# Kernel optimization log

Measured on AMD Instinct MI355X. Metric: run time of the kernel, lower is better.

The kernel has to match this reference:

```python
import jax, jax.numpy as jnp
import numpy as np

B, S, Hd, NH, FF = 4, 2048, 1024, 16, 4096
D = Hd // NH  # head size 64
EPS = 1e-12


def _ln(x, g, b):
    mu = jnp.mean(x, axis=-1, keepdims=True)
    var = jnp.mean(jnp.square(x - mu), axis=-1, keepdims=True)
    return (x - mu) * jax.lax.rsqrt(var + EPS) * g + b


def _rope(q, k):
    # q,k: [B,NH,S,D]; RoFormer interleaved rotary
    inv = 1.0 / (10000.0 ** (jnp.arange(0, D, 2, dtype=jnp.float32) / D))
    freqs = jnp.arange(S, dtype=jnp.float32)[:, None] * inv[None, :]  # [S,D/2]
    cos = jnp.repeat(jnp.cos(freqs), 2, axis=-1)  # [S,D]
    sin = jnp.repeat(jnp.sin(freqs), 2, axis=-1)

    def rot(x):  # [x0,x1,x2,x3,...] -> [-x1,x0,-x3,x2,...]
        return jnp.stack([-x[..., 1::2], x[..., 0::2]], axis=-1).reshape(x.shape)

    return q * cos + rot(q) * sin, k * cos + rot(k) * sin


def setup_inputs() -> dict:
    key = jax.random.key(0)
    ks = jax.random.split(key, 12)
    s = 0.02
    return {
        "x": jax.random.normal(ks[0], (B, S, Hd), jnp.float32),
        "Wq": jax.random.normal(ks[1], (Hd, Hd), jnp.float32) * s,
        "bq": jnp.zeros((Hd,), jnp.float32),
        "Wk": jax.random.normal(ks[2], (Hd, Hd), jnp.float32) * s,
        "bk": jnp.zeros((Hd,), jnp.float32),
        "Wv": jax.random.normal(ks[3], (Hd, Hd), jnp.float32) * s,
        "bv": jnp.zeros((Hd,), jnp.float32),
        "Wo": jax.random.normal(ks[4], (Hd, Hd), jnp.float32) * s,
        "bo": jnp.zeros((Hd,), jnp.float32),
        "g1": jnp.ones((Hd,), jnp.float32),
        "beta1": jnp.zeros((Hd,), jnp.float32),
        "W1": jax.random.normal(ks[5], (Hd, FF), jnp.float32) * s,
        "b1": jnp.zeros((FF,), jnp.float32),
        "W2": jax.random.normal(ks[6], (FF, Hd), jnp.float32) * s,
        "b2": jnp.zeros((Hd,), jnp.float32),
        "g2": jnp.ones((Hd,), jnp.float32),
        "beta2": jnp.zeros((Hd,), jnp.float32),
    }


def reference(x, Wq, bq, Wk, bk, Wv, bv, Wo, bo, g1, beta1, W1, b1, W2, b2, g2, beta2):
    def proj(W, b):  # [B,S,Hd] -> [B,NH,S,D]
        return (x @ W + b).reshape(B, S, NH, D).transpose(0, 2, 1, 3)

    q, k, v = proj(Wq, bq), proj(Wk, bk), proj(Wv, bv)
    q, k = _rope(q, k)
    scores = jnp.einsum('bhqd,bhkd->bhqk', q, k) / jnp.sqrt(jnp.float32(D))
    attn = jax.nn.softmax(scores, axis=-1)
    ctx = jnp.einsum('bhqk,bhkd->bhqd', attn, v)
    ctx = ctx.transpose(0, 2, 1, 3).reshape(B, S, Hd)
    attn_out = ctx @ Wo + bo
    h = _ln(x + attn_out, g1, beta1)
    ffn = jax.nn.gelu(h @ W1 + b1) @ W2 + b2
    return _ln(h + ffn, g2, beta2)
```

## Files before the change

### kernel.cpp

```cpp
#include <hip/hip_runtime.h>

#define BB   4
#define SS   2048
#define HD   1024
#define NHH  16
#define DD   64
#define FFF  4096
#define BS   (BB*SS)
#define BHN  (BB*NHH)

typedef __attribute__((ext_vector_type(8))) short v8s;
typedef __attribute__((ext_vector_type(4))) short v4s;
typedef __attribute__((ext_vector_type(4))) float v4f;

__device__ __forceinline__ short f2bf(float f) {
    union { float f; unsigned u; } v; v.f = f;
    unsigned r = (v.u + 0x7fffu + ((v.u >> 16) & 1u)) >> 16;
    return (short)r;
}
__device__ __forceinline__ float bf2f(short s) {
    union { unsigned u; float f; } v; v.u = ((unsigned)(unsigned short)s) << 16;
    return v.f;
}
__device__ __forceinline__ unsigned pktrunc(float lo, float hi) {
    return __builtin_amdgcn_perm(__builtin_bit_cast(unsigned, hi),
                                 __builtin_bit_cast(unsigned, lo), 0x07060302u);
}
__device__ __forceinline__ v4f mfma16(v8s a, v8s b, v4f c) {
    return __builtin_amdgcn_mfma_f32_16x16x32_bf16(a, b, c, 0, 0, 0);
}
__device__ __forceinline__ void cp16(void* lds, const void* g) {
    __builtin_amdgcn_global_load_lds(
        (const __attribute__((address_space(1))) unsigned*)g,
        (__attribute__((address_space(3))) unsigned*)lds, 16, 0, 0);
}


__global__ __launch_bounds__(256) void cast_bf16(const float* __restrict__ X,
                                                 short* __restrict__ Y, int n) {
    const int i = (blockIdx.x * 256 + threadIdx.x) * 4;
    if (i < n) {
        const float4 v = *(const float4*)(X + i);
        v4s o = { f2bf(v.x), f2bf(v.y), f2bf(v.z), f2bf(v.w) };
        *(v4s*)(Y + i) = o;
    }
}

__global__ __launch_bounds__(256) void rope_tab(float* __restrict__ C, float* __restrict__ Sn) {
    const int i = blockIdx.x * 256 + threadIdx.x;
    const int s = i >> 5, di = i & 31;
    const float inv = powf(10000.f, -(float)(2 * di) * (1.f / 64.f));
    const float a = (float)s * inv;
    C[i]  = cosf(a);
    Sn[i] = sinf(a);
}

__global__ __launch_bounds__(256) void transW(const float* __restrict__ W,
                                              short* __restrict__ WT, int K, int N) {
    __shared__ float T[64][65];
    const int t = threadIdx.x;
    const int r0 = blockIdx.y * 64, c0 = blockIdx.x * 64;
#pragma unroll
    for (int i = 0; i < 4; i++) {
        const int lin = t + 256 * i;
        const int r = lin >> 4, c = (lin & 15) * 4;
        const float4 v = *(const float4*)(W + (size_t)(r0 + r) * N + c0 + c);
        T[r][c] = v.x; T[r][c+1] = v.y; T[r][c+2] = v.z; T[r][c+3] = v.w;
    }
    __syncthreads();
#pragma unroll
    for (int i = 0; i < 4; i++) {
        const int lin = t + 256 * i;
        const int n = lin >> 4, k = (lin & 15) * 4;
        v4s o = { f2bf(T[k][n]), f2bf(T[k+1][n]), f2bf(T[k+2][n]), f2bf(T[k+3][n]) };
        *(v4s*)(WT + (size_t)(c0 + n) * K + r0 + k) = o;
    }
}


template <int EPI>
__global__ __launch_bounds__(256, 2) void gemm_bt(
    const short* __restrict__ A, const short* __restrict__ Bt,
    const float* __restrict__ bias, const float* __restrict__ bias2,
    const float* __restrict__ bias3, void* __restrict__ out,
    void* __restrict__ out2,
    const float* __restrict__ ropeC, const float* __restrict__ ropeS,
    int M, int N, int K, float oscale)
{
    __shared__ short As[128 * 32];
    __shared__ short Bs[128 * 32];
    const int t = threadIdx.x;
    const int wave = t >> 6, lane = t & 63;
    const int quad = lane >> 4, l16 = lane & 15;
    const int wm = wave & 1, wn = wave >> 1;
    const int m0 = blockIdx.x * 128, n0 = blockIdx.y * 128;

    v4f acc[4][4];
#pragma unroll
    for (int i = 0; i < 4; i++)
#pragma unroll
        for (int j = 0; j < 4; j++) { v4f z = {0.f, 0.f, 0.f, 0.f}; acc[i][j] = z; }

    const int r4 = lane >> 2;
    const int g4 = (lane & 3) ^ ((lane >> 3) & 3);
    const short* Asrc = A  + (size_t)(m0 + wave * 32 + r4) * K + g4 * 8;
    const short* Bsrc = Bt + (size_t)(n0 + wave * 32 + r4) * K + g4 * 8;
    short* Adst = As + wave * 1024;
    short* Bdst = Bs + wave * 1024;
    const int pshift = (l16 >> 1) & 3;

    for (int k0 = 0; k0 < K; k0 += 32) {
        __syncthreads();
        cp16(Adst,       Asrc + k0);
        cp16(Adst + 512, Asrc + (size_t)16 * K + k0);
        cp16(Bdst,       Bsrc + k0);
        cp16(Bdst + 512, Bsrc + (size_t)16 * K + k0);
        __syncthreads();
        v8s af[4], bfr[4];
#pragma unroll
        for (int i = 0; i < 4; i++)
            af[i] = *(const v8s*)(As + (wm * 64 + i * 16 + l16) * 32 + (quad ^ pshift) * 8);
#pragma unroll
        for (int j = 0; j < 4; j++)
            bfr[j] = *(const v8s*)(Bs + (wn * 64 + j * 16 + l16) * 32 + (quad ^ pshift) * 8);
#pragma unroll
        for (int i = 0; i < 4; i++)
#pragma unroll
            for (int j = 0; j < 4; j++)
                acc[i][j] = mfma16(af[i], bfr[j], acc[i][j]);
    }

#pragma unroll
    for (int j = 0; j < 4; j++) {
        const int col = n0 + wn * 64 + j * 16 + l16;
        if constexpr (EPI == 0) {
            const int h = col >> 10;
            const float* bp = (h == 0) ? bias : ((h == 1) ? bias2 : bias3);
            const float bval = bp[col & 1023];
            const int d = col & 63;
            const int hh = (col >> 6) & 15;
            if (h == 2) {
#pragma unroll
                for (int i = 0; i < 4; i++) {
                    const int row0 = m0 + wm * 64 + i * 16 + quad * 4;
                    const int b_ = row0 >> 11, s0 = row0 & (SS - 1);
                    v4s ov = { f2bf(acc[i][j][0] + bval), f2bf(acc[i][j][1] + bval),
                               f2bf(acc[i][j][2] + bval), f2bf(acc[i][j][3] + bval) };
                    *(v4s*)((short*)out2 + ((size_t)(b_ * NHH + hh) * DD + d) * SS + s0) = ov;
                }
            } else {
#pragma unroll
                for (int i = 0; i < 4; i++) {
#pragma unroll
                    for (int r = 0; r < 4; r++) {
                        const int row = m0 + wm * 64 + i * 16 + quad * 4 + r;
                        float v = acc[i][j][r] + bval;
                        if (h == 0) v *= oscale;
                        const int s = row & (SS - 1);
                        const float cv = ropeC[s * 32 + (d >> 1)];
                        const float sv = ropeS[s * 32 + (d >> 1)];
                        const float partner = __shfl_xor(v, 1);
                        const float o = (d & 1) ? fmaf(v, cv, partner * sv)
                                                : fmaf(v, cv, -partner * sv);
                        const int b_ = row >> 11;
                        ((short*)out)[(size_t)h * (BHN * SS * DD)
                                      + (((size_t)(b_ * NHH + hh)) * SS + s) * DD + d] = f2bf(o);
                    }
                }
            }
        } else {
            const float bval = bias[col];
#pragma unroll
            for (int i = 0; i < 4; i++) {
#pragma unroll
                for (int r = 0; r < 4; r++) {
                    const int row = m0 + wm * 64 + i * 16 + quad * 4 + r;
                    float v = acc[i][j][r] + bval;
                    const float tq = v * v;
                    const float u = v * fmaf(0.035677408136f, tq, 0.7978845608028654f);
                    const float e = __builtin_amdgcn_exp2f(-2.8853900817779268f * u);
                    const float g = v * __builtin_amdgcn_rcpf(1.f + e);
                    ((short*)out)[(size_t)row * N + col] = f2bf(g);
                }
            }
        }
    }
}


template <int EPI>
__global__ __launch_bounds__(256, 2) void gemm64(
    const short* __restrict__ A, const short* __restrict__ Bt,
    const float* __restrict__ bias, float* __restrict__ out,
    const void* __restrict__ resid, int M, int N, int K)
{
    __shared__ short As[128 * 64];
    __shared__ short Bs[64 * 64];
    const int t = threadIdx.x;
    const int wave = t >> 6, lane = t & 63;
    const int quad = lane >> 4, l16 = lane & 15;
    const int wm = wave & 1, wn = wave >> 1;
    const int m0 = blockIdx.x * 128, n0 = blockIdx.y * 64;

    v4f acc[4][2];
#pragma unroll
    for (int i = 0; i < 4; i++)
#pragma unroll
        for (int j = 0; j < 2; j++) { v4f z = {0.f, 0.f, 0.f, 0.f}; acc[i][j] = z; }

    const int r8 = lane >> 3;
    const int g8 = (lane & 7) ^ r8;
    const short* Asrc = A  + (size_t)(m0 + wave * 32 + r8) * K + g8 * 8;
    const short* Bsrc = Bt + (size_t)(n0 + wave * 16 + r8) * K + g8 * 8;
    short* Adst = As + wave * 2048;
    short* Bdst = Bs + wave * 1024;
    const int xsw = l16 & 7;

    for (int k0 = 0; k0 < K; k0 += 64) {
        __syncthreads();
#pragma unroll
        for (int s = 0; s < 4; s++)
            cp16(Adst + s * 512, Asrc + (size_t)(s * 8) * K + k0);
        cp16(Bdst,       Bsrc + k0);
        cp16(Bdst + 512, Bsrc + (size_t)8 * K + k0);
        __syncthreads();
#pragma unroll
        for (int ks = 0; ks < 2; ks++) {
            v8s af[4], bfr[2];
#pragma unroll
            for (int i = 0; i < 4; i++)
                af[i] = *(const v8s*)(As + (wm * 64 + i * 16 + l16) * 64
                                         + ((ks * 4 + quad) ^ xsw) * 8);
#pragma unroll
            for (int j = 0; j < 2; j++)
                bfr[j] = *(const v8s*)(Bs + (wn * 32 + j * 16 + l16) * 64
                                          + ((ks * 4 + quad) ^ xsw) * 8);
#pragma unroll
            for (int i = 0; i < 4; i++)
#pragma unroll
                for (int j = 0; j < 2; j++)
                    acc[i][j] = mfma16(af[i], bfr[j], acc[i][j]);
        }
    }

#pragma unroll
    for (int j = 0; j < 2; j++) {
        const int col = n0 + wn * 32 + j * 16 + l16;
        const float bval = bias[col];
#pragma unroll
        for (int i = 0; i < 4; i++) {
#pragma unroll
            for (int r = 0; r < 4; r++) {
                const int row = m0 + wm * 64 + i * 16 + quad * 4 + r;
                float v = acc[i][j][r] + bval;
                if constexpr (EPI == 2) v += ((const float*)resid)[(size_t)row * N + col];
                else                    v += bf2f(((const short*)resid)[(size_t)row * N + col]);
                out[(size_t)row * N + col] = v;
            }
        }
    }
}

__global__ __launch_bounds__(256, 3) void attn_kernel(
    const short* __restrict__ Qh, const short* __restrict__ Kh,
    const short* __restrict__ Vt, short* __restrict__ ctx)
{
    __shared__ short Ks[64 * 64];
    __shared__ short Vs[64 * 64];
    __shared__ short Ps[4][16 * 88];
    __shared__ float Li[4][32];
    const int bh = blockIdx.x, q0 = blockIdx.y * 128;
    const int t = threadIdx.x, wave = t >> 6, lane = t & 63;
    const int quad = lane >> 4, l16 = lane & 15;

    const short* qp = Qh + ((size_t)bh * SS + q0 + wave * 32 + l16) * DD;
    v8s bq[2][2];
    bq[0][0] = *(const v8s*)(qp + quad * 8);
    bq[0][1] = *(const v8s*)(qp + 32 + quad * 8);
    bq[1][0] = *(const v8s*)(qp + (size_t)16 * DD + quad * 8);
    bq[1][1] = *(const v8s*)(qp + (size_t)16 * DD + 32 + quad * 8);

    v4f o[2][4];
#pragma unroll
    for (int qs = 0; qs < 2; qs++)
#pragma unroll
        for (int c = 0; c < 4; c++) { v4f z = {0.f, 0.f, 0.f, 0.f}; o[qs][c] = z; }
    float li[2] = {0.f, 0.f};

    const short* Kb = Kh + (size_t)bh * SS * DD;
    const short* Vb = Vt + (size_t)bh * DD * SS;
    const int r8 = lane >> 3;
    const int g8 = (lane & 7) ^ (r8 & 7);
    short* Psw = (short*)Ps[wave];
    const int xsw = l16 & 7;

    for (int kt = 0; kt < SS; kt += 64) {
        __syncthreads();
        cp16(Ks + wave * 1024,       Kb + (size_t)(kt + wave * 16 + r8) * DD + g8 * 8);
        cp16(Ks + wave * 1024 + 512, Kb + (size_t)(kt + wave * 16 + 8 + r8) * DD + g8 * 8);
        cp16(Vs + wave * 1024,       Vb + (size_t)(wave * 16 + r8) * SS + kt + g8 * 8);
        cp16(Vs + wave * 1024 + 512, Vb + (size_t)(wave * 16 + 8 + r8) * SS + kt + g8 * 8);
        __syncthreads();

        v4f sc[2][4];
#pragma unroll
        for (int c = 0; c < 4; c++) {
            const v8s k0f = *(const v8s*)(Ks + (c * 16 + l16) * 64 + ((quad    ) ^ xsw) * 8);
            const v8s k1f = *(const v8s*)(Ks + (c * 16 + l16) * 64 + ((quad + 4) ^ xsw) * 8);
#pragma unroll
            for (int qs = 0; qs < 2; qs++) {
                v4f z = {0.f, 0.f, 0.f, 0.f};
                z = mfma16(k0f, bq[qs][0], z);
                z = mfma16(k1f, bq[qs][1], z);
                sc[qs][c] = z;
            }
        }

        v8s pa[2][2];
#pragma unroll
        for (int qs = 0; qs < 2; qs++) {
            float lp = 0.f;
#pragma unroll
            for (int c = 0; c < 4; c++) {
#pragma unroll
                for (int r = 0; r < 4; r++) {
                    const float p = __builtin_amdgcn_exp2f(sc[qs][c][r]);
                    sc[qs][c][r] = p;
                    lp += p;
                }
            }
            li[qs] += lp;
            short* pw = Psw + l16 * 88;
#pragma unroll
            for (int c = 0; c < 4; c++) {
                uint2 w;
                w.x = pktrunc(sc[qs][c][0], sc[qs][c][1]);
                w.y = pktrunc(sc[qs][c][2], sc[qs][c][3]);
                *(uint2*)(pw + c * 16 + quad * 4) = w;
            }
            pa[qs][0] = *(const v8s*)(Psw + l16 * 88 + quad * 8);
            pa[qs][1] = *(const v8s*)(Psw + l16 * 88 + 32 + quad * 8);
        }

#pragma unroll
        for (int c = 0; c < 4; c++) {
            const v8s v0f = *(const v8s*)(Vs + (c * 16 + l16) * 64 + ((quad    ) ^ xsw) * 8);
            const v8s v1f = *(const v8s*)(Vs + (c * 16 + l16) * 64 + ((quad + 4) ^ xsw) * 8);
#pragma unroll
            for (int qs = 0; qs < 2; qs++) {
                o[qs][c] = mfma16(pa[qs][0], v0f, o[qs][c]);
                o[qs][c] = mfma16(pa[qs][1], v1f, o[qs][c]);
            }
        }
    }

    float linv[2][4];
#pragma unroll
    for (int qs = 0; qs < 2; qs++) {
        float lf = li[qs];
        lf += __shfl_xor(lf, 16);
        lf += __shfl_xor(lf, 32);
        if (quad == 0) Li[wave][qs * 16 + l16] = lf;
    }
    __syncthreads();
#pragma unroll
    for (int qs = 0; qs < 2; qs++) {
        const v4f lv = *(const v4f*)(&Li[wave][qs * 16 + quad * 4]);
#pragma unroll
        for (int r = 0; r < 4; r++) linv[qs][r] = __builtin_amdgcn_rcpf(lv[r]);
    }
    const int b_ = bh >> 4, h_ = bh & 15;
#pragma unroll
    for (int qs = 0; qs < 2; qs++)
#pragma unroll
        for (int c = 0; c < 4; c++)
#pragma unroll
            for (int r = 0; r < 4; r++) {
                const int s = q0 + wave * 32 + qs * 16 + quad * 4 + r;
                const int d = c * 16 + l16;
                ctx[((size_t)(b_ * SS + s)) * HD + h_ * DD + d] =
                    f2bf(o[qs][c][r] * linv[qs][r]);
            }
}

__global__ __launch_bounds__(256) void ln_kernel(
    const float* __restrict__ X, const float* __restrict__ g, const float* __restrict__ b,
    float* __restrict__ Y, short* __restrict__ Yb)
{
    const int row = blockIdx.x;
    const int t = threadIdx.x;
    const float4 v = *(const float4*)(X + (size_t)row * HD + t * 4);
    float s = v.x + v.y + v.z + v.w;
    float sq = v.x * v.x + v.y * v.y + v.z * v.z + v.w * v.w;
#pragma unroll
    for (int m = 1; m < 64; m <<= 1) { s += __shfl_xor(s, m); sq += __shfl_xor(sq, m); }
    __shared__ float red[8];
    const int wave = t >> 6, lane = t & 63;
    if (lane == 0) { red[wave] = s; red[4 + wave] = sq; }
    __syncthreads();
    s  = red[0] + red[1] + red[2] + red[3];
    sq = red[4] + red[5] + red[6] + red[7];
    const float mu = s * (1.f / HD);
    const float var = sq * (1.f / HD) - mu * mu;
    const float rs = rsqrtf(var + 1e-12f);
    const float4 gg = *(const float4*)(g + t * 4);
    const float4 bb = *(const float4*)(b + t * 4);
    const float y0 = (v.x - mu) * rs * gg.x + bb.x;
    const float y1 = (v.y - mu) * rs * gg.y + bb.y;
    const float y2 = (v.z - mu) * rs * gg.z + bb.z;
    const float y3 = (v.w - mu) * rs * gg.w + bb.w;
    if (Y)  { float4 o = { y0, y1, y2, y3 }; *(float4*)(Y + (size_t)row * HD + t * 4) = o; }
    if (Yb) { v4s o = { f2bf(y0), f2bf(y1), f2bf(y2), f2bf(y3) };
              *(v4s*)(Yb + (size_t)row * HD + t * 4) = o; }
}

extern "C" void kernel_launch(void* const* d_in, const int* in_sizes, int n_in,
                              void* d_out, int out_size, void* d_ws, size_t ws_size,
                              hipStream_t stream)
{
    (void)in_sizes; (void)n_in; (void)out_size;
    const float* x   = (const float*)d_in[0];
    const float* Wq  = (const float*)d_in[1];
    const float* bq  = (const float*)d_in[2];
    const float* Wk  = (const float*)d_in[3];
    const float* bk  = (const float*)d_in[4];
    const float* Wv  = (const float*)d_in[5];
    const float* bv  = (const float*)d_in[6];
    const float* Wo  = (const float*)d_in[7];
    const float* bo  = (const float*)d_in[8];
    const float* g1  = (const float*)d_in[9];
    const float* be1 = (const float*)d_in[10];
    const float* W1  = (const float*)d_in[11];
    const float* b1  = (const float*)d_in[12];
    const float* W2  = (const float*)d_in[13];
    const float* b2  = (const float*)d_in[14];
    const float* g2  = (const float*)d_in[15];
    const float* be2 = (const float*)d_in[16];

    char* ws = (char*)d_ws;
    size_t off = 0;
    auto alloc = [&](size_t sz) { char* p = ws + off; off += sz; return p; };
    short* xb    = (short*)alloc((size_t)BS * HD * 2);
    short* WqkvT = (short*)alloc((size_t)3 * HD * HD * 2);
    short* WoT   = (short*)alloc((size_t)HD * HD * 2);
    short* W1T   = (short*)alloc((size_t)FFF * HD * 2);
    short* W2T   = (short*)alloc((size_t)HD * FFF * 2);
    float* ropeC = (float*)alloc((size_t)SS * 32 * 4);
    float* ropeS = (float*)alloc((size_t)SS * 32 * 4);
    short* Qh    = (short*)alloc((size_t)BHN * SS * DD * 2);
    short* Kh    = (short*)alloc((size_t)BHN * SS * DD * 2);
    short* Vt    = (short*)alloc((size_t)BHN * SS * DD * 2);
    short* ctx   = (short*)alloc((size_t)BS * HD * 2);
    float* ao    = (float*)alloc((size_t)BS * HD * 4);
    if (off > ws_size) return;
    short* f1 = Qh;
    short* hb = xb;
    float* f2 = (float*)d_out;

    const float qsc = 0.125f * 1.4426950408889634f;

    cast_bf16<<<BS * HD / 1024, 256, 0, stream>>>(x, xb, BS * HD);
    rope_tab<<<SS * 32 / 256, 256, 0, stream>>>(ropeC, ropeS);
    transW<<<dim3(16, 16), 256, 0, stream>>>(Wq, WqkvT, HD, HD);
    transW<<<dim3(16, 16), 256, 0, stream>>>(Wk, WqkvT + (size_t)HD * HD, HD, HD);
    transW<<<dim3(16, 16), 256, 0, stream>>>(Wv, WqkvT + (size_t)2 * HD * HD, HD, HD);
    transW<<<dim3(16, 16), 256, 0, stream>>>(Wo, WoT, HD, HD);
    transW<<<dim3(64, 16), 256, 0, stream>>>(W1, W1T, HD, FFF);
    transW<<<dim3(16, 64), 256, 0, stream>>>(W2, W2T, FFF, HD);

    gemm_bt<0><<<dim3(64, 24), 256, 0, stream>>>(xb, WqkvT, bq, bk, bv, Qh, Vt,
                                                 ropeC, ropeS, BS, 3 * HD, HD, qsc);
    attn_kernel<<<dim3(64, SS / 128), 256, 0, stream>>>(Qh, Kh, Vt, ctx);
    gemm64<2><<<dim3(64, 16), 256, 0, stream>>>(ctx, WoT, bo, ao, x, BS, HD, HD);
    ln_kernel<<<BS, 256, 0, stream>>>(ao, g1, be1, nullptr, hb);
    gemm_bt<3><<<dim3(64, 32), 256, 0, stream>>>(hb, W1T, b1, nullptr, nullptr, f1, nullptr,
                                                 nullptr, nullptr, BS, FFF, HD, 1.0f);
    gemm64<4><<<dim3(64, 16), 256, 0, stream>>>(f1, W2T, b2, f2, hb, BS, HD, FFF);
    ln_kernel<<<BS, 256, 0, stream>>>(f2, g2, be2, (float*)d_out, nullptr);
}
```

Before: 515.8 us.

## Replace QKV and FFN1 GEMMs with 256x256 double-buffered 8-wave pipelined kernel

Replaces the 128x128 single-buffered GEMM used for the QKV and FFN-up projections with a 256x256 tile kernel of 8 waves. It double-buffers LDS over 64-wide K steps and interleaves async global-to-LDS copies with MFMA phases, using explicit barriers, s_setprio and vmcnt waits. The aim is to hide load latency and raise arithmetic intensity per byte loaded. In exchange it uses more LDS and accumulator registers, which may lower occupancy, and the grids become smaller (384 and 512 blocks), which may underfill the CUs.

```diff
diff --git a/kernel.cpp b/kernel.cpp
--- a/kernel.cpp
+++ b/kernel.cpp
@@ -78,8 +78,32 @@
 }
 
 
+#define GPHASE(BUF, MH, KS, READB, STAGE_CALL, DOVM)                             \
+  {                                                                              \
+    v8s af[4];                                                                   \
+    _Pragma("unroll")                                                            \
+    for (int i2 = 0; i2 < 4; i2++)                                               \
+      af[i2] = *(const v8s*)&As[BUF][KS][wm*128 + (MH)*64 + i2*16 + l16][co];    \
+    if (READB) {                                                                 \
+      _Pragma("unroll")                                                          \
+      for (int j = 0; j < 4; j++)                                                \
+        bfr[j] = *(const v8s*)&Bs[BUF][KS][wn*64 + j*16 + l16][co];              \
+    }                                                                            \
+    STAGE_CALL;                                                                  \
+    asm volatile("s_barrier" ::: "memory");                                      \
+    __builtin_amdgcn_s_setprio(1);                                               \
+    _Pragma("unroll")                                                            \
+    for (int i2 = 0; i2 < 4; i2++)                                               \
+      _Pragma("unroll")                                                          \
+      for (int j = 0; j < 4; j++)                                                \
+        acc[(MH)*4+i2][j] = mfma16(af[i2], bfr[j], acc[(MH)*4+i2][j]);           \
+    __builtin_amdgcn_s_setprio(0);                                               \
+    if (DOVM) asm volatile("s_waitcnt vmcnt(4)" ::: "memory");                   \
+    asm volatile("s_barrier" ::: "memory");                                      \
+  }
+
 template <int EPI>
-__global__ __launch_bounds__(256, 2) void gemm_bt(
+__global__ __launch_bounds__(512, 2) void gemm8p(
     const short* __restrict__ A, const short* __restrict__ Bt,
     const float* __restrict__ bias, const float* __restrict__ bias2,
     const float* __restrict__ bias3, void* __restrict__ out,
@@ -87,48 +111,55 @@
     const float* __restrict__ ropeC, const float* __restrict__ ropeS,
     int M, int N, int K, float oscale)
 {
-    __shared__ short As[128 * 32];
-    __shared__ short Bs[128 * 32];
+    __shared__ short As[2][2][256][32];
+    __shared__ short Bs[2][2][256][32];
     const int t = threadIdx.x;
     const int wave = t >> 6, lane = t & 63;
     const int quad = lane >> 4, l16 = lane & 15;
-    const int wm = wave & 1, wn = wave >> 1;
-    const int m0 = blockIdx.x * 128, n0 = blockIdx.y * 128;
-
-    v4f acc[4][4];
-#pragma unroll
-    for (int i = 0; i < 4; i++)
+    const int wm = wave >> 2, wn = wave & 3;
+    const int m0 = blockIdx.x * 256, n0 = blockIdx.y * 256;
+
+    v4f acc[8][4];
+#pragma unroll
+    for (int i = 0; i < 8; i++)
 #pragma unroll
         for (int j = 0; j < 4; j++) { v4f z = {0.f, 0.f, 0.f, 0.f}; acc[i][j] = z; }
 
-    const int r4 = lane >> 2;
-    const int g4 = (lane & 3) ^ ((lane >> 3) & 3);
-    const short* Asrc = A  + (size_t)(m0 + wave * 32 + r4) * K + g4 * 8;
-    const short* Bsrc = Bt + (size_t)(n0 + wave * 32 + r4) * K + g4 * 8;
-    short* Adst = As + wave * 1024;
-    short* Bdst = Bs + wave * 1024;
-    const int pshift = (l16 >> 1) & 3;
-
-    for (int k0 = 0; k0 < K; k0 += 32) {
-        __syncthreads();
-        cp16(Adst,       Asrc + k0);
-        cp16(Adst + 512, Asrc + (size_t)16 * K + k0);
-        cp16(Bdst,       Bsrc + k0);
-        cp16(Bdst + 512, Bsrc + (size_t)16 * K + k0);
-        __syncthreads();
-        v8s af[4], bfr[4];
-#pragma unroll
-        for (int i = 0; i < 4; i++)
-            af[i] = *(const v8s*)(As + (wm * 64 + i * 16 + l16) * 32 + (quad ^ pshift) * 8);
-#pragma unroll
-        for (int j = 0; j < 4; j++)
-            bfr[j] = *(const v8s*)(Bs + (wn * 64 + j * 16 + l16) * 32 + (quad ^ pshift) * 8);
-#pragma unroll
-        for (int i = 0; i < 4; i++)
-#pragma unroll
-            for (int j = 0; j < 4; j++)
-                acc[i][j] = mfma16(af[i], bfr[j], acc[i][j]);
-    }
+    const int r16 = lane >> 2;
+    const int g4  = (lane & 3) ^ ((r16 >> 1) & 3);
+    const short* Ag = A  + (size_t)(m0 + wave * 32 + r16) * K + g4 * 8;
+    const short* Bg = Bt + (size_t)(n0 + wave * 32 + r16) * K + g4 * 8;
+    const int co = (quad ^ ((l16 >> 1) & 3)) * 8;
+
+    auto stageA = [&](int buf, int ks, int kofs) {
+        cp16(&As[buf][ks][wave * 32][0],      Ag + kofs + ks * 32);
+        cp16(&As[buf][ks][wave * 32 + 16][0], Ag + (size_t)16 * K + kofs + ks * 32);
+    };
+    auto stageB = [&](int buf, int ks, int kofs) {
+        cp16(&Bs[buf][ks][wave * 32][0],      Bg + kofs + ks * 32);
+        cp16(&Bs[buf][ks][wave * 32 + 16][0], Bg + (size_t)16 * K + kofs + ks * 32);
+    };
+
+    stageA(0, 0, 0); stageB(0, 0, 0);
+    stageA(0, 1, 0); stageB(0, 1, 0);
+    asm volatile("s_waitcnt vmcnt(0)" ::: "memory");
+    __syncthreads();
+
+    v8s bfr[4];
+    const int NT = K >> 6;
+    for (int it = 0; it < (NT >> 1); it++) {
+        const int kA = (2 * it + 1) * 64;
+        const int kB = (2 * it + 2) < NT ? (2 * it + 2) * 64 : (K - 64);
+        GPHASE(0, 0, 0, true,  stageA(1, 0, kA), false)
+        GPHASE(0, 1, 0, false, stageB(1, 0, kA), true)
+        GPHASE(0, 0, 1, true,  stageA(1, 1, kA), false)
+        GPHASE(0, 1, 1, false, stageB(1, 1, kA), true)
+        GPHASE(1, 0, 0, true,  stageA(0, 0, kB), false)
+        GPHASE(1, 1, 0, false, stageB(0, 0, kB), true)
+        GPHASE(1, 0, 1, true,  stageA(0, 1, kB), false)
+        GPHASE(1, 1, 1, false, stageB(0, 1, kB), true)
+    }
+    asm volatile("s_waitcnt vmcnt(0)" ::: "memory");
 
 #pragma unroll
     for (int j = 0; j < 4; j++) {
@@ -141,8 +172,8 @@
             const int hh = (col >> 6) & 15;
             if (h == 2) {
 #pragma unroll
-                for (int i = 0; i < 4; i++) {
-                    const int row0 = m0 + wm * 64 + i * 16 + quad * 4;
+                for (int i = 0; i < 8; i++) {
+                    const int row0 = m0 + wm * 128 + i * 16 + quad * 4;
                     const int b_ = row0 >> 11, s0 = row0 & (SS - 1);
                     v4s ov = { f2bf(acc[i][j][0] + bval), f2bf(acc[i][j][1] + bval),
                                f2bf(acc[i][j][2] + bval), f2bf(acc[i][j][3] + bval) };
@@ -150,10 +181,10 @@
                 }
             } else {
 #pragma unroll
-                for (int i = 0; i < 4; i++) {
+                for (int i = 0; i < 8; i++) {
 #pragma unroll
                     for (int r = 0; r < 4; r++) {
-                        const int row = m0 + wm * 64 + i * 16 + quad * 4 + r;
+                        const int row = m0 + wm * 128 + i * 16 + quad * 4 + r;
                         float v = acc[i][j][r] + bval;
                         if (h == 0) v *= oscale;
                         const int s = row & (SS - 1);
@@ -171,10 +202,10 @@
         } else {
             const float bval = bias[col];
 #pragma unroll
-            for (int i = 0; i < 4; i++) {
+            for (int i = 0; i < 8; i++) {
 #pragma unroll
                 for (int r = 0; r < 4; r++) {
-                    const int row = m0 + wm * 64 + i * 16 + quad * 4 + r;
+                    const int row = m0 + wm * 128 + i * 16 + quad * 4 + r;
                     float v = acc[i][j][r] + bval;
                     const float tq = v * v;
                     const float u = v * fmaf(0.035677408136f, tq, 0.7978845608028654f);
@@ -468,13 +499,13 @@
     transW<<<dim3(64, 16), 256, 0, stream>>>(W1, W1T, HD, FFF);
     transW<<<dim3(16, 64), 256, 0, stream>>>(W2, W2T, FFF, HD);
 
-    gemm_bt<0><<<dim3(64, 24), 256, 0, stream>>>(xb, WqkvT, bq, bk, bv, Qh, Vt,
-                                                 ropeC, ropeS, BS, 3 * HD, HD, qsc);
+    gemm8p<0><<<dim3(32, 12), 512, 0, stream>>>(xb, WqkvT, bq, bk, bv, Qh, Vt,
+                                                ropeC, ropeS, BS, 3 * HD, HD, qsc);
     attn_kernel<<<dim3(64, SS / 128), 256, 0, stream>>>(Qh, Kh, Vt, ctx);
     gemm64<2><<<dim3(64, 16), 256, 0, stream>>>(ctx, WoT, bo, ao, x, BS, HD, HD);
     ln_kernel<<<BS, 256, 0, stream>>>(ao, g1, be1, nullptr, hb);
-    gemm_bt<3><<<dim3(64, 32), 256, 0, stream>>>(hb, W1T, b1, nullptr, nullptr, f1, nullptr,
-                                                 nullptr, nullptr, BS, FFF, HD, 1.0f);
+    gemm8p<3><<<dim3(32, 16), 512, 0, stream>>>(hb, W1T, b1, nullptr, nullptr, f1, nullptr,
+                                                nullptr, nullptr, BS, FFF, HD, 1.0f);
     gemm64<4><<<dim3(64, 16), 256, 0, stream>>>(f1, W2T, b2, f2, hb, BS, HD, FFF);
     ln_kernel<<<BS, 256, 0, stream>>>(f2, g2, be2, (float*)d_out, nullptr);
 }
```

Result: slower. 542.4 us (+5.2%).

## Unify GEMMs into 128x128 tile kernel with BK=64 and raise attention occupancy

Applied to the files above, without the earlier changes.

Replaces the 128x32-K gemm_bt and the 128x64 gemm64 with one gemm128 kernel using 128x128 output tiles and a 64-wide K step with XOR swizzle. The residual-add epilogues move into this kernel, so the Wo and W2 projections run with half as many blocks and twice the reuse per tile. It also raises the attention kernel's launch-bounds occupancy hint from 3 to 4. This aims to cut barrier count and global/LDS traffic per FLOP, at the cost of more shared memory per block and possible register pressure or spills in attention.

```diff
diff --git a/kernel.cpp b/kernel.cpp
--- a/kernel.cpp
+++ b/kernel.cpp
@@ -79,16 +79,16 @@
 
 
 template <int EPI>
-__global__ __launch_bounds__(256, 2) void gemm_bt(
+__global__ __launch_bounds__(256, 2) void gemm128(
     const short* __restrict__ A, const short* __restrict__ Bt,
     const float* __restrict__ bias, const float* __restrict__ bias2,
     const float* __restrict__ bias3, void* __restrict__ out,
-    void* __restrict__ out2,
+    void* __restrict__ out2, const void* __restrict__ resid,
     const float* __restrict__ ropeC, const float* __restrict__ ropeS,
     int M, int N, int K, float oscale)
 {
-    __shared__ short As[128 * 32];
-    __shared__ short Bs[128 * 32];
+    __shared__ short As[128 * 64];
+    __shared__ short Bs[128 * 64];
     const int t = threadIdx.x;
     const int wave = t >> 6, lane = t & 63;
     const int quad = lane >> 4, l16 = lane & 15;
@@ -101,33 +101,39 @@
 #pragma unroll
         for (int j = 0; j < 4; j++) { v4f z = {0.f, 0.f, 0.f, 0.f}; acc[i][j] = z; }
 
-    const int r4 = lane >> 2;
-    const int g4 = (lane & 3) ^ ((lane >> 3) & 3);
-    const short* Asrc = A  + (size_t)(m0 + wave * 32 + r4) * K + g4 * 8;
-    const short* Bsrc = Bt + (size_t)(n0 + wave * 32 + r4) * K + g4 * 8;
-    short* Adst = As + wave * 1024;
-    short* Bdst = Bs + wave * 1024;
-    const int pshift = (l16 >> 1) & 3;
-
-    for (int k0 = 0; k0 < K; k0 += 32) {
+    const int r8 = lane >> 3;
+    const int g8 = (lane & 7) ^ r8;
+    const short* Asrc = A  + (size_t)(m0 + wave * 32 + r8) * K + g8 * 8;
+    const short* Bsrc = Bt + (size_t)(n0 + wave * 32 + r8) * K + g8 * 8;
+    short* Adst = As + wave * 2048;
+    short* Bdst = Bs + wave * 2048;
+    const int xsw = l16 & 7;
+
+    for (int k0 = 0; k0 < K; k0 += 64) {
         __syncthreads();
-        cp16(Adst,       Asrc + k0);
-        cp16(Adst + 512, Asrc + (size_t)16 * K + k0);
-        cp16(Bdst,       Bsrc + k0);
-        cp16(Bdst + 512, Bsrc + (size_t)16 * K + k0);
+#pragma unroll
+        for (int s = 0; s < 4; s++) {
+            cp16(Adst + s * 512, Asrc + (size_t)(s * 8) * K + k0);
+            cp16(Bdst + s * 512, Bsrc + (size_t)(s * 8) * K + k0);
+        }
         __syncthreads();
-        v8s af[4], bfr[4];
-#pragma unroll
-        for (int i = 0; i < 4; i++)
-            af[i] = *(const v8s*)(As + (wm * 64 + i * 16 + l16) * 32 + (quad ^ pshift) * 8);
-#pragma unroll
-        for (int j = 0; j < 4; j++)
-            bfr[j] = *(const v8s*)(Bs + (wn * 64 + j * 16 + l16) * 32 + (quad ^ pshift) * 8);
-#pragma unroll
-        for (int i = 0; i < 4; i++)
+#pragma unroll
+        for (int ks = 0; ks < 2; ks++) {
+            v8s af[4], bfr[4];
+#pragma unroll
+            for (int i = 0; i < 4; i++)
+                af[i] = *(const v8s*)(As + (wm * 64 + i * 16 + l16) * 64
+                                         + ((ks * 4 + quad) ^ xsw) * 8);
 #pragma unroll
             for (int j = 0; j < 4; j++)
-                acc[i][j] = mfma16(af[i], bfr[j], acc[i][j]);
+                bfr[j] = *(const v8s*)(Bs + (wn * 64 + j * 16 + l16) * 64
+                                          + ((ks * 4 + quad) ^ xsw) * 8);
+#pragma unroll
+            for (int i = 0; i < 4; i++)
+#pragma unroll
+                for (int j = 0; j < 4; j++)
+                    acc[i][j] = mfma16(af[i], bfr[j], acc[i][j]);
+        }
     }
 
 #pragma unroll
@@ -168,7 +174,7 @@
                     }
                 }
             }
-        } else {
+        } else if constexpr (EPI == 3) {
             const float bval = bias[col];
 #pragma unroll
             for (int i = 0; i < 4; i++) {
@@ -183,85 +189,24 @@
                     ((short*)out)[(size_t)row * N + col] = f2bf(g);
                 }
             }
-        }
-    }
-}
-
-
-template <int EPI>
-__global__ __launch_bounds__(256, 2) void gemm64(
-    const short* __restrict__ A, const short* __restrict__ Bt,
-    const float* __restrict__ bias, float* __restrict__ out,
-    const void* __restrict__ resid, int M, int N, int K)
-{
-    __shared__ short As[128 * 64];
-    __shared__ short Bs[64 * 64];
-    const int t = threadIdx.x;
-    const int wave = t >> 6, lane = t & 63;
-    const int quad = lane >> 4, l16 = lane & 15;
-    const int wm = wave & 1, wn = wave >> 1;
-    const int m0 = blockIdx.x * 128, n0 = blockIdx.y * 64;
-
-    v4f acc[4][2];
-#pragma unroll
-    for (int i = 0; i < 4; i++)
-#pragma unroll
-        for (int j = 0; j < 2; j++) { v4f z = {0.f, 0.f, 0.f, 0.f}; acc[i][j] = z; }
-
-    const int r8 = lane >> 3;
-    const int g8 = (lane & 7) ^ r8;
-    const short* Asrc = A  + (size_t)(m0 + wave * 32 + r8) * K + g8 * 8;
-    const short* Bsrc = Bt + (size_t)(n0 + wave * 16 + r8) * K + g8 * 8;
-    short* Adst = As + wave * 2048;
-    short* Bdst = Bs + wave * 1024;
-    const int xsw = l16 & 7;
-
-    for (int k0 = 0; k0 < K; k0 += 64) {
-        __syncthreads();
-#pragma unroll
-        for (int s = 0; s < 4; s++)
-            cp16(Adst + s * 512, Asrc + (size_t)(s * 8) * K + k0);
-        cp16(Bdst,       Bsrc + k0);
-        cp16(Bdst + 512, Bsrc + (size_t)8 * K + k0);
-        __syncthreads();
-#pragma unroll
-        for (int ks = 0; ks < 2; ks++) {
-            v8s af[4], bfr[2];
-#pragma unroll
-            for (int i = 0; i < 4; i++)
-                af[i] = *(const v8s*)(As + (wm * 64 + i * 16 + l16) * 64
-                                         + ((ks * 4 + quad) ^ xsw) * 8);
-#pragma unroll
-            for (int j = 0; j < 2; j++)
-                bfr[j] = *(const v8s*)(Bs + (wn * 32 + j * 16 + l16) * 64
-                                          + ((ks * 4 + quad) ^ xsw) * 8);
-#pragma unroll
-            for (int i = 0; i < 4; i++)
-#pragma unroll
-                for (int j = 0; j < 2; j++)
-                    acc[i][j] = mfma16(af[i], bfr[j], acc[i][j]);
-        }
-    }
-
-#pragma unroll
-    for (int j = 0; j < 2; j++) {
-        const int col = n0 + wn * 32 + j * 16 + l16;
-        const float bval = bias[col];
-#pragma unroll
-        for (int i = 0; i < 4; i++) {
-#pragma unroll
-            for (int r = 0; r < 4; r++) {
-                const int row = m0 + wm * 64 + i * 16 + quad * 4 + r;
-                float v = acc[i][j][r] + bval;
-                if constexpr (EPI == 2) v += ((const float*)resid)[(size_t)row * N + col];
-                else                    v += bf2f(((const short*)resid)[(size_t)row * N + col]);
-                out[(size_t)row * N + col] = v;
-            }
-        }
-    }
-}
-
-__global__ __launch_bounds__(256, 3) void attn_kernel(
+        } else {
+            const float bval = bias[col];
+#pragma unroll
+            for (int i = 0; i < 4; i++) {
+#pragma unroll
+                for (int r = 0; r < 4; r++) {
+                    const int row = m0 + wm * 64 + i * 16 + quad * 4 + r;
+                    float v = acc[i][j][r] + bval;
+                    if constexpr (EPI == 2) v += ((const float*)resid)[(size_t)row * N + col];
+                    else                    v += bf2f(((const short*)resid)[(size_t)row * N + col]);
+                    ((float*)out)[(size_t)row * N + col] = v;
+                }
+            }
+        }
+    }
+}
+
+__global__ __launch_bounds__(256, 4) void attn_kernel(
     const short* __restrict__ Qh, const short* __restrict__ Kh,
     const short* __restrict__ Vt, short* __restrict__ ctx)
 {
@@ -468,13 +413,15 @@
     transW<<<dim3(64, 16), 256, 0, stream>>>(W1, W1T, HD, FFF);
     transW<<<dim3(16, 64), 256, 0, stream>>>(W2, W2T, FFF, HD);
 
-    gemm_bt<0><<<dim3(64, 24), 256, 0, stream>>>(xb, WqkvT, bq, bk, bv, Qh, Vt,
-                                                 ropeC, ropeS, BS, 3 * HD, HD, qsc);
+    gemm128<0><<<dim3(64, 24), 256, 0, stream>>>(xb, WqkvT, bq, bk, bv, Qh, Vt,
+                                                 nullptr, ropeC, ropeS, BS, 3 * HD, HD, qsc);
     attn_kernel<<<dim3(64, SS / 128), 256, 0, stream>>>(Qh, Kh, Vt, ctx);
-    gemm64<2><<<dim3(64, 16), 256, 0, stream>>>(ctx, WoT, bo, ao, x, BS, HD, HD);
+    gemm128<2><<<dim3(64, 8), 256, 0, stream>>>(ctx, WoT, bo, nullptr, nullptr, ao,
+                                                nullptr, x, nullptr, nullptr, BS, HD, HD, 1.0f);
     ln_kernel<<<BS, 256, 0, stream>>>(ao, g1, be1, nullptr, hb);
-    gemm_bt<3><<<dim3(64, 32), 256, 0, stream>>>(hb, W1T, b1, nullptr, nullptr, f1, nullptr,
-                                                 nullptr, nullptr, BS, FFF, HD, 1.0f);
-    gemm64<4><<<dim3(64, 16), 256, 0, stream>>>(f1, W2T, b2, f2, hb, BS, HD, FFF);
+    gemm128<3><<<dim3(64, 32), 256, 0, stream>>>(hb, W1T, b1, nullptr, nullptr, f1,
+                                                 nullptr, nullptr, nullptr, nullptr, BS, FFF, HD, 1.0f);
+    gemm128<4><<<dim3(64, 8), 256, 0, stream>>>(f1, W2T, b2, nullptr, nullptr, f2,
+                                                nullptr, hb, nullptr, nullptr, BS, HD, FFF, 1.0f);
     ln_kernel<<<BS, 256, 0, stream>>>(f2, g2, be2, (float*)d_out, nullptr);
 }
```

Result: faster. 505.1 us (-2.1%).
